# Kernel optimization log

Hardware: AMD Instinct MI355X
Metric: run time of the kernel (lower is better)

Reference implementation:

```python
import jax, jax.numpy as jnp
import numpy as np

N = 50_000      # nodes
E = 1_600_000   # edges (avg degree 32)
IN = 128        # in_channels
H = 128         # hidden_channels
OUT = 10        # out_channels
EA = 16         # edge_attr_channels


def setup_inputs() -> dict:
    key = jax.random.key(0)
    ks = jax.random.split(key, 16)
    def lin(k, fan_in, fan_out):
        return jax.random.normal(k, (fan_in, fan_out), dtype=jnp.float32) * (1.0 / np.sqrt(fan_in))
    return {
        "x": jax.random.normal(ks[0], (N, IN), dtype=jnp.float32),
        "edge_index": jax.random.randint(ks[1], (2, E), 0, N, dtype=jnp.int32),
        "edge_attr": jax.random.normal(ks[2], (E, EA), dtype=jnp.float32),
        # edge encoder MLP: Linear(EA->H) -> ReLU -> Linear(H->1)
        "We1": lin(ks[3], EA, H), "be1": jnp.zeros((H,), jnp.float32),
        "We2": lin(ks[4], H, 1),  "be2": jnp.zeros((1,), jnp.float32),
        # three GCNConv layers (in->H, H->H, H->H)
        "W1": lin(ks[5], IN, H), "b1": jnp.zeros((H,), jnp.float32),
        "W2": lin(ks[6], H, H),  "b2": jnp.zeros((H,), jnp.float32),
        "W3": lin(ks[7], H, H),  "b3": jnp.zeros((H,), jnp.float32),
        # head Linear(H->OUT)
        "Wh": lin(ks[8], H, OUT), "bh": jnp.zeros((OUT,), jnp.float32),
    }


def reference(x, edge_index, edge_attr, We1, be1, We2, be2,
              W1, b1, W2, b2, W3, b3, Wh, bh):
    n = x.shape[0]
    src, dst = edge_index[0], edge_index[1]

    # edge weight = softplus(MLP(edge_attr)).squeeze(-1)
    hidden = jax.nn.relu(edge_attr @ We1 + be1)          # [E, H]
    ew = jax.nn.softplus((hidden @ We2 + be2)[:, 0])      # [E]

    # add self-loops with weight 1 (GCNConv default)
    loops = jnp.arange(n, dtype=src.dtype)
    src_f = jnp.concatenate([src, loops])
    dst_f = jnp.concatenate([dst, loops])
    w_f = jnp.concatenate([ew, jnp.ones((n,), ew.dtype)])

    # symmetric normalization: D^{-1/2} A D^{-1/2}
    deg = jax.ops.segment_sum(w_f, dst_f, num_segments=n)   # [N]
    dis = jax.lax.rsqrt(jnp.maximum(deg, 1e-12))
    norm = dis[src_f] * w_f * dis[dst_f]                     # [E+N]

    def gcn_conv(h, W, b):
        h = h @ W                                             # [N, H]
        msg = norm[:, None] * h[src_f]                        # gather + scale
        agg = jax.ops.segment_sum(msg, dst_f, num_segments=n) # scatter-add
        return agg + b

    h = jax.nn.relu(gcn_conv(x, W1, b1))   # dropout is identity in eval
    h = jax.nn.relu(gcn_conv(h, W2, b2))
    h = jax.nn.relu(gcn_conv(h, W3, b3))

    graph_emb = jnp.mean(h, axis=0)        # global mean pool (single graph)
    return graph_emb @ Wh + bh             # [OUT], already squeezed
```

## Files before the change

kernel.cpp:

```cpp
#include <hip/hip_runtime.h>


#define HD   128
#define EAD  16
#define OUTD 10
#define PCHUNK 4096
#define PBLK 400

typedef short bf16x8 __attribute__((ext_vector_type(8)));
typedef float f32x16 __attribute__((ext_vector_type(16)));

static inline int ceil_div(long long a, long long b){ return (int)((a + b - 1) / b); }

__device__ inline unsigned f2bf(float f) {
    unsigned u = __float_as_uint(f);
    return (u + 0x7fffu + ((u >> 16) & 1u)) >> 16;
}
__device__ inline float bf_lo(unsigned w) { return __uint_as_float(w << 16); }
__device__ inline float bf_hi(unsigned w) { return __uint_as_float(w & 0xffff0000u); }

__device__ inline unsigned short f2h(float f) {
    _Float16 h = (_Float16)f;
    return __builtin_bit_cast(unsigned short, h);
}
__device__ inline float h2f(unsigned u) {
    _Float16 h = __builtin_bit_cast(_Float16, (unsigned short)(u & 0xffffu));
    return (float)h;
}
__device__ inline unsigned cvtpk(float lo, float hi) {
    unsigned r;
    asm volatile("v_cvt_pk_bf16_f32 %0, %1, %2" : "=v"(r) : "v"(lo), "v"(hi));
    return r;
}
__device__ inline unsigned relu_pk(unsigned w) {
    return w & ~(((w >> 15) & 0x10001u) * 0xFFFFu);
}

__global__ __launch_bounds__(256) void k_edge_mlp(
    const float* __restrict__ edge_attr,
    const float* __restrict__ We1, const float* __restrict__ be1,
    const float* __restrict__ We2, const float* __restrict__ be2,
    float* __restrict__ ew, int E)
{
    const int lane = threadIdx.x & 63;
    const int half = lane >> 5;
    const int lc   = lane & 31;
    const int wid  = blockIdx.x * 4 + (threadIdx.x >> 6);
    const int nw   = gridDim.x * 4;
    const int G    = (E + 31) >> 5;

    bf16x8 bfr[4];
    float  we2v[4], be1v[4];
#pragma unroll
    for (int t = 0; t < 4; ++t) {
#pragma unroll
        for (int j = 0; j < 8; ++j) {
            int krow = 4 * half + (j & 3) + 8 * (j >> 2);
            bfr[t][j] = (short)f2bf(We1[krow * HD + t * 32 + lc]);
        }
        we2v[t] = We2[t * 32 + lc];
        be1v[t] = be1[t * 32 + lc];
    }
    const float be2v = be2[0];

    for (int g = wid; g < G; g += nw) {
        int eb = g << 5;
        int edge = eb + lc;
        int eload = edge < E ? edge : E - 1;
        const float4* rowp = reinterpret_cast<const float4*>(edge_attr + (size_t)eload * EAD);
        float4 a0 = rowp[half];
        float4 a1 = rowp[2 + half];
        bf16x8 af;
        af[0] = (short)f2bf(a0.x); af[1] = (short)f2bf(a0.y);
        af[2] = (short)f2bf(a0.z); af[3] = (short)f2bf(a0.w);
        af[4] = (short)f2bf(a1.x); af[5] = (short)f2bf(a1.y);
        af[6] = (short)f2bf(a1.z); af[7] = (short)f2bf(a1.w);

        f32x16 acc0, acc1, acc2, acc3;
#pragma unroll
        for (int i = 0; i < 16; ++i) { acc0[i]=0.f; acc1[i]=0.f; acc2[i]=0.f; acc3[i]=0.f; }
        acc0 = __builtin_amdgcn_mfma_f32_32x32x16_bf16(af, bfr[0], acc0, 0, 0, 0);
        acc1 = __builtin_amdgcn_mfma_f32_32x32x16_bf16(af, bfr[1], acc1, 0, 0, 0);
        acc2 = __builtin_amdgcn_mfma_f32_32x32x16_bf16(af, bfr[2], acc2, 0, 0, 0);
        acc3 = __builtin_amdgcn_mfma_f32_32x32x16_bf16(af, bfr[3], acc3, 0, 0, 0);

        float p[16];
#pragma unroll
        for (int r = 0; r < 16; ++r) {
            float s;
            s = fmaxf(acc0[r] + be1v[0], 0.f) * we2v[0];
            s = fmaf(fmaxf(acc1[r] + be1v[1], 0.f), we2v[1], s);
            s = fmaf(fmaxf(acc2[r] + be1v[2], 0.f), we2v[2], s);
            s = fmaf(fmaxf(acc3[r] + be1v[3], 0.f), we2v[3], s);
            p[r] = s;
        }
#pragma unroll
        for (int r = 0; r < 16; ++r) {
#pragma unroll
            for (int off = 1; off < 32; off <<= 1)
                p[r] += __shfl_xor(p[r], off, 64);
        }
        if (lc < 16) {
            int q = lc;
            float mine = p[0];
#pragma unroll
            for (int r = 1; r < 16; ++r) mine = (q == r) ? p[r] : mine;
            int row = (q & 3) + 8 * (q >> 2) + 4 * half;
            int e2 = eb + row;
            if (e2 < E) {
                float v  = mine + be2v;
                ew[e2] = fmaxf(v, 0.f) + log1pf(expf(-fabsf(v)));
            }
        }
    }
}

__global__ __launch_bounds__(256) void k_bcount(
    const int* __restrict__ dst, int* __restrict__ batom, int E, int NB)
{
    __shared__ int hist[256];
    int t = threadIdx.x;
    hist[t] = 0;
    __syncthreads();
    int base = blockIdx.x * PCHUNK;
#pragma unroll
    for (int k = 0; k < PCHUNK / 256; ++k) {
        int e = base + k * 256 + t;
        if (e < E) atomicAdd(&hist[dst[e] >> 8], 1);
    }
    __syncthreads();
    if (t < NB && hist[t]) atomicAdd(&batom[t], hist[t]);
}

__global__ __launch_bounds__(256) void k_bscan(
    const int* __restrict__ batom, int* __restrict__ boff,
    int* __restrict__ bcur, int NB)
{
    __shared__ int sh[256];
    int t = threadIdx.x;
    int v = (t < NB) ? batom[t] : 0;
    sh[t] = v;
    __syncthreads();
    for (int off = 1; off < 256; off <<= 1) {
        int add = (t >= off) ? sh[t - off] : 0;
        __syncthreads();
        sh[t] += add;
        __syncthreads();
    }
    if (t < NB) { boff[t] = sh[t] - v; bcur[t] = sh[t] - v; }
    if (t == NB - 1) boff[NB] = sh[t];
}

__global__ __launch_bounds__(256) void k_part(
    const int* __restrict__ src, const int* __restrict__ dst,
    const float* __restrict__ ew, int* __restrict__ bcur,
    uint2* __restrict__ bbuf, int E, int NB)
{
    __shared__ int hist[256];
    __shared__ int base[256];
    __shared__ int cur[256];
    int t = threadIdx.x;
    hist[t] = 0; cur[t] = 0;
    __syncthreads();
    int eb = blockIdx.x * PCHUNK;
#pragma unroll
    for (int k = 0; k < PCHUNK / 256; ++k) {
        int e = eb + k * 256 + t;
        if (e < E) atomicAdd(&hist[dst[e] >> 8], 1);
    }
    __syncthreads();
    if (t < NB && hist[t]) base[t] = atomicAdd(&bcur[t], hist[t]);
    __syncthreads();
#pragma unroll
    for (int k = 0; k < PCHUNK / 256; ++k) {
        int e = eb + k * 256 + t;
        if (e >= E) continue;
        int d = dst[e];
        int bkt = d >> 8;
        int pos = base[bkt] + atomicAdd(&cur[bkt], 1);
        bbuf[pos] = make_uint2(((unsigned)src[e] << 16) | f2h(ew[e]),
                               (unsigned)(d & 255));
    }
}

__global__ __launch_bounds__(256) void k_bucket(
    const int* __restrict__ boff, const uint2* __restrict__ bbuf,
    int* __restrict__ rp, float* __restrict__ dis,
    unsigned* __restrict__ adj, int N, int E, int NB)
{
    __shared__ int   hcnt[256];
    __shared__ int   hexc[256];
    __shared__ int   cur[256];
    __shared__ float degs[256];
    int b = blockIdx.x;
    int t = threadIdx.x;
    hcnt[t] = 0; cur[t] = 0; degs[t] = 0.f;
    __syncthreads();
    int beg = boff[b], end = boff[b + 1];
    for (int i = beg + t; i < end; i += 256) {
        uint2 ent = bbuf[i];
        int dl = (int)ent.y;
        atomicAdd(&hcnt[dl], 1);
        atomicAdd(&degs[dl], h2f(ent.x));
    }
    __syncthreads();
    {
        int v = hcnt[t];
        hexc[t] = v;
        __syncthreads();
        for (int off = 1; off < 256; off <<= 1) {
            int add = (t >= off) ? hexc[t - off] : 0;
            __syncthreads();
            hexc[t] += add;
            __syncthreads();
        }
        hexc[t] -= v;
    }
    int n = (b << 8) + t;
    if (n < N) {
        rp[n]  = beg + hexc[t];
        dis[n] = rsqrtf(fmaxf(1.0f + degs[t], 1e-12f));
    }
    if (b == NB - 1 && t == 0) rp[N] = E;
    __syncthreads();
    for (int i = beg + t; i < end; i += 256) {
        uint2 ent = bbuf[i];
        int dl = (int)ent.y;
        int pos = beg + hexc[dl] + atomicAdd(&cur[dl], 1);
        adj[pos] = ent.x;
    }
}

template <bool BF16IN, bool RELU>
__global__ __launch_bounds__(256) void k_gemm(
    const void* __restrict__ Xv, const float* __restrict__ W,
    const float* __restrict__ dis, unsigned short* __restrict__ Ybf, int N)
{
    __shared__ unsigned short Wt[128][132];
    int t = threadIdx.x;
#pragma unroll
    for (int i = 0; i < 64; ++i) {
        int e = i * 256 + t;
        int k = e >> 7, n = e & 127;
        Wt[n][k] = (unsigned short)f2bf(W[e]);
    }
    __syncthreads();

    const int lane = t & 63;
    const int half = lane >> 5;
    const int lc   = lane & 31;
    const int wid  = blockIdx.x * 4 + (t >> 6);
    const int nw   = gridDim.x * 4;
    const int T    = (N + 31) >> 5;

    for (int tile = wid; tile < T; tile += nw) {
        int rbase = tile << 5;
        int arow  = rbase + lc; if (arow >= N) arow = N - 1;

        f32x16 acc[4];
#pragma unroll
        for (int tb = 0; tb < 4; ++tb)
#pragma unroll
            for (int i = 0; i < 16; ++i) acc[tb][i] = 0.f;

#pragma unroll
        for (int kk = 0; kk < 8; ++kk) {
            union { uint2 u[2]; bf16x8 v; } af;
            if (BF16IN) {
                const unsigned short* Xb = (const unsigned short*)Xv;
                const unsigned short* rp = Xb + (size_t)arow * HD + kk * 16 + 4 * half;
                uint2 lo = *reinterpret_cast<const uint2*>(rp);
                uint2 hi = *reinterpret_cast<const uint2*>(rp + 8);
                if (RELU) {
                    lo.x = relu_pk(lo.x); lo.y = relu_pk(lo.y);
                    hi.x = relu_pk(hi.x); hi.y = relu_pk(hi.y);
                }
                af.u[0] = lo; af.u[1] = hi;
            } else {
                const float* Xf = (const float*)Xv;
                const float* rp = Xf + (size_t)arow * HD + kk * 16 + 4 * half;
                float4 lo = *reinterpret_cast<const float4*>(rp);
                float4 hi = *reinterpret_cast<const float4*>(rp + 8);
                af.u[0] = make_uint2(cvtpk(lo.x, lo.y), cvtpk(lo.z, lo.w));
                af.u[1] = make_uint2(cvtpk(hi.x, hi.y), cvtpk(hi.z, hi.w));
            }
#pragma unroll
            for (int tb = 0; tb < 4; ++tb) {
                const unsigned short* wp = &Wt[tb * 32 + lc][kk * 16 + 4 * half];
                union { uint2 u[2]; bf16x8 v; } bf_;
                bf_.u[0] = *reinterpret_cast<const uint2*>(wp);
                bf_.u[1] = *reinterpret_cast<const uint2*>(wp + 8);
                acc[tb] = __builtin_amdgcn_mfma_f32_32x32x16_bf16(af.v, bf_.v, acc[tb], 0, 0, 0);
            }
        }

        float disv = dis[arow];
#pragma unroll
        for (int r = 0; r < 16; ++r) {
            int rofs = (r & 3) + 8 * (r >> 2) + 4 * half;
            int grow = rbase + rofs;
            float d = __shfl(disv, rofs, 32);
            if (grow < N) {
#pragma unroll
                for (int tb = 0; tb < 4; ++tb)
                    Ybf[(size_t)grow * HD + tb * 32 + lc] =
                        (unsigned short)f2bf(acc[tb][r] * d);
            }
        }
    }
}

__global__ __launch_bounds__(256) void k_gather(
    const int* __restrict__ rp, const unsigned* __restrict__ adj,
    const unsigned* __restrict__ linbf, const float* __restrict__ dis,
    const float* __restrict__ b, unsigned short* __restrict__ out, int N)
{
    int n = blockIdx.x * 8 + (threadIdx.x >> 5);
    if (n >= N) return;
    int lane = threadIdx.x & 31;
    uint2 sw = *reinterpret_cast<const uint2*>(linbf + (size_t)n * (HD/2) + lane * 2);
    float4 acc;
    acc.x = bf_lo(sw.x); acc.y = bf_hi(sw.x);
    acc.z = bf_lo(sw.y); acc.w = bf_hi(sw.y);
    int beg = rp[n], end = rp[n + 1];
    for (int i0 = beg; i0 < end; i0 += 32) {
        int m = end - i0; if (m > 32) m = 32;
        unsigned a = 0;
        if (lane < m) a = adj[i0 + lane];
        int j = 0;
        for (; j + 8 <= m; j += 8) {
            unsigned ee[8]; uint2 vv[8];
#pragma unroll
            for (int q = 0; q < 8; ++q) ee[q] = __shfl(a, j + q, 32);
#pragma unroll
            for (int q = 0; q < 8; ++q)
                vv[q] = *reinterpret_cast<const uint2*>(linbf + (size_t)(ee[q] >> 16) * (HD/2) + lane * 2);
#pragma unroll
            for (int q = 0; q < 8; ++q) {
                float wq = h2f(ee[q]);
                acc.x = fmaf(wq, bf_lo(vv[q].x), acc.x);
                acc.y = fmaf(wq, bf_hi(vv[q].x), acc.y);
                acc.z = fmaf(wq, bf_lo(vv[q].y), acc.z);
                acc.w = fmaf(wq, bf_hi(vv[q].y), acc.w);
            }
        }
        for (; j < m; ++j) {
            unsigned e0 = __shfl(a, j, 32);
            uint2 v0 = *reinterpret_cast<const uint2*>(linbf + (size_t)(e0 >> 16) * (HD/2) + lane * 2);
            float w0 = h2f(e0);
            acc.x = fmaf(w0, bf_lo(v0.x), acc.x);
            acc.y = fmaf(w0, bf_hi(v0.x), acc.y);
            acc.z = fmaf(w0, bf_lo(v0.y), acc.z);
            acc.w = fmaf(w0, bf_hi(v0.y), acc.w);
        }
    }
    float dn = dis[n];
    float4 bv = reinterpret_cast<const float4*>(b)[lane];
    unsigned w0 = cvtpk(fmaf(dn, acc.x, bv.x), fmaf(dn, acc.y, bv.y));
    unsigned w1 = cvtpk(fmaf(dn, acc.z, bv.z), fmaf(dn, acc.w, bv.w));
    *reinterpret_cast<uint2*>(out + (size_t)n * HD + lane * 4) = make_uint2(w0, w1);
}

__global__ __launch_bounds__(256) void k_pool(
    const unsigned short* __restrict__ h, float* __restrict__ part, int N)
{
    __shared__ float sm[16][128];
    int t  = threadIdx.x;
    int cg = t & 15;
    int rs = t >> 4;
    float acc[8];
#pragma unroll
    for (int i = 0; i < 8; ++i) acc[i] = 0.f;
    for (int r = blockIdx.x * 16 + rs; r < N; r += gridDim.x * 16) {
        uint4 v = *reinterpret_cast<const uint4*>(h + (size_t)r * HD + cg * 8);
        acc[0] += fmaxf(bf_lo(v.x), 0.f);
        acc[1] += fmaxf(bf_hi(v.x), 0.f);
        acc[2] += fmaxf(bf_lo(v.y), 0.f);
        acc[3] += fmaxf(bf_hi(v.y), 0.f);
        acc[4] += fmaxf(bf_lo(v.z), 0.f);
        acc[5] += fmaxf(bf_hi(v.z), 0.f);
        acc[6] += fmaxf(bf_lo(v.w), 0.f);
        acc[7] += fmaxf(bf_hi(v.w), 0.f);
    }
#pragma unroll
    for (int i = 0; i < 8; ++i) sm[rs][cg * 8 + i] = acc[i];
    __syncthreads();
    if (t < 128) {
        float s = 0.f;
#pragma unroll
        for (int k = 0; k < 16; ++k) s += sm[k][t];
        part[blockIdx.x * HD + t] = s;
    }
}

__global__ __launch_bounds__(1024) void k_head(
    const float* __restrict__ part, const float* __restrict__ Wh,
    const float* __restrict__ bh, float* __restrict__ out, float invN)
{
    __shared__ float smc[8][128];
    __shared__ float col[HD];
    int t = threadIdx.x;
    {
        int c  = t & 127;
        int ch = t >> 7;
        float s0 = 0.f, s1 = 0.f;
        int k0 = ch * 50;
#pragma unroll
        for (int k = 0; k < 50; k += 2) {
            s0 += part[(k0 + k)     * HD + c];
            s1 += part[(k0 + k + 1) * HD + c];
        }
        smc[ch][c] = s0 + s1;
    }
    __syncthreads();
    if (t < 128) {
        float s = 0.f;
#pragma unroll
        for (int k = 0; k < 8; ++k) s += smc[k][t];
        col[t] = s * invN;
    }
    __syncthreads();
    {
        int o = t >> 6;
        int l = t & 63;
        if (o < OUTD) {
            float acc = col[l] * Wh[l * OUTD + o]
                      + col[l + 64] * Wh[(l + 64) * OUTD + o];
#pragma unroll
            for (int off = 1; off < 64; off <<= 1)
                acc += __shfl_xor(acc, off, 64);
            if (l == 0) out[o] = acc + bh[o];
        }
    }
}

extern "C" void kernel_launch(void* const* d_in, const int* in_sizes, int n_in,
                              void* d_out, int out_size, void* d_ws, size_t ws_size,
                              hipStream_t stream)
{
    const float* x         = (const float*)d_in[0];
    const int*   ei        = (const int*)  d_in[1];
    const float* edge_attr = (const float*)d_in[2];
    const float* We1       = (const float*)d_in[3];
    const float* be1       = (const float*)d_in[4];
    const float* We2       = (const float*)d_in[5];
    const float* be2       = (const float*)d_in[6];
    const float* W1        = (const float*)d_in[7];
    const float* b1        = (const float*)d_in[8];
    const float* W2        = (const float*)d_in[9];
    const float* b2        = (const float*)d_in[10];
    const float* W3        = (const float*)d_in[11];
    const float* b3        = (const float*)d_in[12];
    const float* Wh        = (const float*)d_in[13];
    const float* bh        = (const float*)d_in[14];

    const int N = in_sizes[0] / HD;
    const int E = in_sizes[2] / EAD;
    const int NB = (N + 255) >> 8;
    const int* srcp = ei;
    const int* dstp = ei + E;

    char* w = (char*)d_ws;
    float*          ew   = (float*)w;          w += (size_t)E * sizeof(float);
    float*          dis  = (float*)w;          w += (size_t)N * sizeof(float);
    unsigned short* Bbf  = (unsigned short*)w; w += (size_t)N * HD * sizeof(unsigned short);
    unsigned*       Abf  = (unsigned*)w;       w += (size_t)N * (HD/2) * sizeof(unsigned);
    float*          part = (float*)w;          w += (size_t)PBLK * HD * sizeof(float);
    int*            rp   = (int*)w;            w += (size_t)(N + 2) * sizeof(int);
    int*            batom= (int*)w;            w += 256 * sizeof(int);
    int*            boff = (int*)w;            w += 260 * sizeof(int);
    int*            bcur = (int*)w;            w += 256 * sizeof(int);
    w = (char*)(((uintptr_t)w + 15) & ~(uintptr_t)15);
    uint2*          bbuf = (uint2*)w;          w += (size_t)E * sizeof(uint2);
    unsigned*       adj  = (unsigned*)w;       w += (size_t)E * sizeof(unsigned);

    const int gGe   = ceil_div(N, 8);
    const int gPart = ceil_div(E, PCHUNK);
    const int gGemm = 196;

    k_edge_mlp<<<1024, 256, 0, stream>>>(edge_attr, We1, be1, We2, be2, ew, E);

    hipMemsetAsync(batom, 0, 256 * sizeof(int), stream);
    k_bcount<<<gPart, 256, 0, stream>>>(dstp, batom, E, NB);
    k_bscan <<<1, 256, 0, stream>>>(batom, boff, bcur, NB);
    k_part  <<<gPart, 256, 0, stream>>>(srcp, dstp, ew, bcur, bbuf, E, NB);
    k_bucket<<<NB, 256, 0, stream>>>(boff, bbuf, rp, dis, adj, N, E, NB);

    k_gemm<false, false><<<gGemm, 256, 0, stream>>>(x, W1, dis, (unsigned short*)Abf, N);
    k_gather<<<gGe, 256, 0, stream>>>(rp, adj, Abf, dis, b1, Bbf, N);
    k_gemm<true, true><<<gGemm, 256, 0, stream>>>(Bbf, W2, dis, (unsigned short*)Abf, N);
    k_gather<<<gGe, 256, 0, stream>>>(rp, adj, Abf, dis, b2, Bbf, N);
    k_gemm<true, true><<<gGemm, 256, 0, stream>>>(Bbf, W3, dis, (unsigned short*)Abf, N);
    k_gather<<<gGe, 256, 0, stream>>>(rp, adj, Abf, dis, b3, Bbf, N);

    k_pool<<<PBLK, 256, 0, stream>>>(Bbf, part, N);
    k_head<<<1, 1024, 0, stream>>>(part, Wh, bh, (float*)d_out, 1.0f / (float)N);
}
```

Measured before the change: 392.9 us.

## Fuse bucket histogram into edge MLP and compute second layer via MFMA

The destination-bucket histogram kernel is folded into the edge-MLP kernel, so dst is read there and one launch disappears. The edge MLP is reorganised into a transposed MFMA formulation: the bias is added through an extra MFMA against a ones vector, the hidden activations are ReLU'd and packed to bf16, and the H->1 projection becomes further MFMAs. This replaces the many cross-lane shuffle reductions per edge group. In exchange the hidden activations and We2 are rounded to bf16, which adds precision loss to the edge weights.

New measurement: 376.8 us. -4.1%, faster.

```diff
diff --git a/kernel.cpp b/kernel.cpp
--- a/kernel.cpp
+++ b/kernel.cpp
@@ -37,99 +37,90 @@
 }
 
 __global__ __launch_bounds__(256) void k_edge_mlp(
-    const float* __restrict__ edge_attr,
+    const float* __restrict__ edge_attr, const int* __restrict__ dst,
     const float* __restrict__ We1, const float* __restrict__ be1,
     const float* __restrict__ We2, const float* __restrict__ be2,
-    float* __restrict__ ew, int E)
-{
-    const int lane = threadIdx.x & 63;
+    float* __restrict__ ew, int* __restrict__ batom, int E, int NB)
+{
+    __shared__ int hist[256];
+    const int tid = threadIdx.x;
+    hist[tid] = 0;
+    __syncthreads();
+
+    const int lane = tid & 63;
     const int half = lane >> 5;
     const int lc   = lane & 31;
-    const int wid  = blockIdx.x * 4 + (threadIdx.x >> 6);
+    const int wid  = blockIdx.x * 4 + (tid >> 6);
     const int nw   = gridDim.x * 4;
     const int G    = (E + 31) >> 5;
 
     bf16x8 bfr[4];
-    float  we2v[4], be1v[4];
+    bf16x8 abias[4];
+    bf16x8 bones;
+    bf16x8 we2A[8];
 #pragma unroll
     for (int t = 0; t < 4; ++t) {
 #pragma unroll
         for (int j = 0; j < 8; ++j) {
-            int krow = 4 * half + (j & 3) + 8 * (j >> 2);
-            bfr[t][j] = (short)f2bf(We1[krow * HD + t * 32 + lc]);
-        }
-        we2v[t] = We2[t * 32 + lc];
-        be1v[t] = be1[t * 32 + lc];
-    }
+            int k = 4 * half + (j & 3) + 8 * (j >> 2);
+            bfr[t][j]   = (short)f2bf(We1[k * HD + t * 32 + lc]);
+            abias[t][j] = (half == 0 && j == 0) ? (short)f2bf(be1[t * 32 + lc]) : (short)0;
+        }
+    }
+#pragma unroll
+    for (int j = 0; j < 8; ++j)
+        bones[j] = (half == 0 && j == 0) ? (short)0x3F80 : (short)0;
+#pragma unroll
+    for (int s = 0; s < 8; ++s)
+#pragma unroll
+        for (int j = 0; j < 8; ++j) {
+            int k = 4 * half + (j & 3) + 8 * (j >> 2);
+            we2A[s][j] = (short)f2bf(We2[s * 16 + k]);
+        }
     const float be2v = be2[0];
 
     for (int g = wid; g < G; g += nw) {
         int eb = g << 5;
         int edge = eb + lc;
         int eload = edge < E ? edge : E - 1;
+        bool owner = (half == 0) && (edge < E);
+        if (owner) atomicAdd(&hist[((unsigned)dst[edge]) >> 8], 1);
+
         const float4* rowp = reinterpret_cast<const float4*>(edge_attr + (size_t)eload * EAD);
         float4 a0 = rowp[half];
         float4 a1 = rowp[2 + half];
-        bf16x8 af;
-        af[0] = (short)f2bf(a0.x); af[1] = (short)f2bf(a0.y);
-        af[2] = (short)f2bf(a0.z); af[3] = (short)f2bf(a0.w);
-        af[4] = (short)f2bf(a1.x); af[5] = (short)f2bf(a1.y);
-        af[6] = (short)f2bf(a1.z); af[7] = (short)f2bf(a1.w);
-
-        f32x16 acc0, acc1, acc2, acc3;
-#pragma unroll
-        for (int i = 0; i < 16; ++i) { acc0[i]=0.f; acc1[i]=0.f; acc2[i]=0.f; acc3[i]=0.f; }
-        acc0 = __builtin_amdgcn_mfma_f32_32x32x16_bf16(af, bfr[0], acc0, 0, 0, 0);
-        acc1 = __builtin_amdgcn_mfma_f32_32x32x16_bf16(af, bfr[1], acc1, 0, 0, 0);
-        acc2 = __builtin_amdgcn_mfma_f32_32x32x16_bf16(af, bfr[2], acc2, 0, 0, 0);
-        acc3 = __builtin_amdgcn_mfma_f32_32x32x16_bf16(af, bfr[3], acc3, 0, 0, 0);
-
-        float p[16];
-#pragma unroll
-        for (int r = 0; r < 16; ++r) {
-            float s;
-            s = fmaxf(acc0[r] + be1v[0], 0.f) * we2v[0];
-            s = fmaf(fmaxf(acc1[r] + be1v[1], 0.f), we2v[1], s);
-            s = fmaf(fmaxf(acc2[r] + be1v[2], 0.f), we2v[2], s);
-            s = fmaf(fmaxf(acc3[r] + be1v[3], 0.f), we2v[3], s);
-            p[r] = s;
-        }
-#pragma unroll
-        for (int r = 0; r < 16; ++r) {
-#pragma unroll
-            for (int off = 1; off < 32; off <<= 1)
-                p[r] += __shfl_xor(p[r], off, 64);
-        }
-        if (lc < 16) {
-            int q = lc;
-            float mine = p[0];
-#pragma unroll
-            for (int r = 1; r < 16; ++r) mine = (q == r) ? p[r] : mine;
-            int row = (q & 3) + 8 * (q >> 2) + 4 * half;
-            int e2 = eb + row;
-            if (e2 < E) {
-                float v  = mine + be2v;
-                ew[e2] = fmaxf(v, 0.f) + log1pf(expf(-fabsf(v)));
-            }
-        }
-    }
-}
-
-__global__ __launch_bounds__(256) void k_bcount(
-    const int* __restrict__ dst, int* __restrict__ batom, int E, int NB)
-{
-    __shared__ int hist[256];
-    int t = threadIdx.x;
-    hist[t] = 0;
-    __syncthreads();
-    int base = blockIdx.x * PCHUNK;
-#pragma unroll
-    for (int k = 0; k < PCHUNK / 256; ++k) {
-        int e = base + k * 256 + t;
-        if (e < E) atomicAdd(&hist[dst[e] >> 8], 1);
-    }
-    __syncthreads();
-    if (t < NB && hist[t]) atomicAdd(&batom[t], hist[t]);
+        union { uint2 u[2]; bf16x8 v; } af;
+        af.u[0] = make_uint2(cvtpk(a0.x, a0.y), cvtpk(a0.z, a0.w));
+        af.u[1] = make_uint2(cvtpk(a1.x, a1.y), cvtpk(a1.z, a1.w));
+
+        f32x16 pre;
+#pragma unroll
+        for (int i = 0; i < 16; ++i) pre[i] = 0.f;
+#pragma unroll
+        for (int t = 0; t < 4; ++t) {
+            f32x16 acc;
+#pragma unroll
+            for (int i = 0; i < 16; ++i) acc[i] = 0.f;
+            acc = __builtin_amdgcn_mfma_f32_32x32x16_bf16(abias[t], bones, acc, 0, 0, 0);
+            acc = __builtin_amdgcn_mfma_f32_32x32x16_bf16(bfr[t], af.v, acc, 0, 0, 0);
+            union { uint2 u[2]; bf16x8 v; } plo, phi;
+            plo.u[0] = make_uint2(cvtpk(fmaxf(acc[0], 0.f),  fmaxf(acc[1], 0.f)),
+                                  cvtpk(fmaxf(acc[2], 0.f),  fmaxf(acc[3], 0.f)));
+            plo.u[1] = make_uint2(cvtpk(fmaxf(acc[4], 0.f),  fmaxf(acc[5], 0.f)),
+                                  cvtpk(fmaxf(acc[6], 0.f),  fmaxf(acc[7], 0.f)));
+            phi.u[0] = make_uint2(cvtpk(fmaxf(acc[8], 0.f),  fmaxf(acc[9], 0.f)),
+                                  cvtpk(fmaxf(acc[10], 0.f), fmaxf(acc[11], 0.f)));
+            phi.u[1] = make_uint2(cvtpk(fmaxf(acc[12], 0.f), fmaxf(acc[13], 0.f)),
+                                  cvtpk(fmaxf(acc[14], 0.f), fmaxf(acc[15], 0.f)));
+            pre = __builtin_amdgcn_mfma_f32_32x32x16_bf16(we2A[2*t],     plo.v, pre, 0, 0, 0);
+            pre = __builtin_amdgcn_mfma_f32_32x32x16_bf16(we2A[2*t + 1], phi.v, pre, 0, 0, 0);
+        }
+        float v  = pre[0] + be2v;
+        float sp = fmaxf(v, 0.f) + log1pf(expf(-fabsf(v)));
+        if (owner) ew[edge] = sp;
+    }
+    __syncthreads();
+    if (tid < NB && hist[tid]) atomicAdd(&batom[tid], hist[tid]);
 }
 
 __global__ __launch_bounds__(256) void k_bscan(
@@ -478,10 +469,10 @@
     const int gPart = ceil_div(E, PCHUNK);
     const int gGemm = 196;
 
-    k_edge_mlp<<<1024, 256, 0, stream>>>(edge_attr, We1, be1, We2, be2, ew, E);
-
     hipMemsetAsync(batom, 0, 256 * sizeof(int), stream);
-    k_bcount<<<gPart, 256, 0, stream>>>(dstp, batom, E, NB);
+    k_edge_mlp<<<1024, 256, 0, stream>>>(edge_attr, dstp, We1, be1, We2, be2,
+                                         ew, batom, E, NB);
+
     k_bscan <<<1, 256, 0, stream>>>(batom, boff, bcur, NB);
     k_part  <<<gPart, 256, 0, stream>>>(srcp, dstp, ew, bcur, bbuf, E, NB);
     k_bucket<<<NB, 256, 0, stream>>>(boff, bbuf, rp, dis, adj, N, E, NB);
```
